# Kernel optimization log

Hardware: AMD Instinct MI355X
Metric: run time of the kernel (lower is better)

## Reference

```python
import jax, jax.numpy as jnp
import numpy as np
jax.config.update("jax_enable_x64", True)

TAPS, DELAY = 5, 3
EPS = 1e-6        # DNN_WPE.eps: power clamp before WPE
WPE_EPS = 1e-10   # wpe_one_iteration eps: inverse-power clamp + diag loading


def _signal_framing(Y, L):
    # Y: (..., T) -> (..., T-L+1, L) sliding frames (as_strided equivalent)
    T = Y.shape[-1]
    idx = jnp.arange(T - L + 1)[:, None] + jnp.arange(L)[None, :]
    return Y[..., idx]


def _wpe_one_iteration(Y, power, taps, delay):
    # Y: (B,F,C,T) complex128, power: (B,F,T) float64
    B, F, C, T = Y.shape
    inv_power = 1.0 / jnp.maximum(power, WPE_EPS)
    Tp = T - delay - taps + 1
    # tap-stacked delayed signal, taps axis reversed: (B,F,C,Tp,taps)
    Psi = _signal_framing(Y, taps)[..., :Tp, :][..., ::-1]
    Psi_n = Psi.conj() * inv_power[:, :, None, delay + taps - 1:, None]
    # covariance R: (B,F,taps*C,taps*C); cross-corr P: (B,F,taps,C_e,C_d)
    R = jnp.einsum("bfdtk,bfetl->bfkdle", Psi_n, Psi).reshape(B, F, taps * C, taps * C)
    P = jnp.einsum("bfdtk,bfet->bfked", Psi_n, Y[..., delay + taps - 1:])
    # v: (B,F,C_e,taps*C_d); conj filter G = inv(R) @ v^T  (X = v @ inv(R)^T)
    v = P.transpose(0, 1, 3, 2, 4).reshape(B, F, C, taps * C)
    eye = jnp.eye(taps * C, dtype=R.dtype)
    tr = jnp.trace(R, axis1=-2, axis2=-1).real[..., None, None] / (taps * C)
    G = jnp.linalg.solve(R + WPE_EPS * tr * eye, v.transpose(0, 1, 3, 2))
    G = G.reshape(B, F, taps, C, C)  # (B,F,tau,d,e) conjugated filter matrix
    # reverb tail: sum over taps of filtered, delayed signal
    tail = jnp.zeros_like(Y)
    for tau in range(taps):  # taps=5, small fixed loop
        s = delay + tau
        contrib = jnp.einsum("bfde,bfdt->bfet", G[:, :, tau], Y[..., : T - s])
        tail = tail.at[..., s:].add(contrib)
    return Y - tail


def setup_inputs() -> dict:
    key = jax.random.key(0)
    k1, k2, k3 = jax.random.split(key, 3)
    B, T, C, F = 4, 512, 8, 257
    data_real = jax.random.normal(k1, (B, T, C, F), dtype=jnp.float32)
    data_imag = jax.random.normal(k2, (B, T, C, F), dtype=jnp.float32)
    ilens = jax.random.randint(k3, (B,), 256, T + 1)
    return {"data_real": data_real, "data_imag": data_imag, "ilens": ilens}


def reference(data_real, data_imag, ilens):
    # (B,T,C,F) -> (B,F,C,T)
    data = (data_real + 1j * data_imag).transpose(0, 3, 2, 1)
    # power averaged over channels, clamped (B,F,T)
    power = jnp.maximum(jnp.mean(data.real ** 2 + data.imag ** 2, axis=-2), EPS)
    enh = _wpe_one_iteration(data.astype(jnp.complex128), power.astype(jnp.float64), TAPS, DELAY)
    enh = enh.astype(jnp.complex64)
    T = enh.shape[-1]
    pad = (jnp.arange(T)[None, :] >= ilens[:, None])[:, None, None, :]  # (B,1,1,T)
    enh = jnp.where(pad, 0.0 + 0.0j, enh)
    enh = enh.transpose(0, 3, 2, 1)  # back to (B,T,C,F)
    return enh.real, enh.imag, power
```

## Files before the change

### kernel.cpp

```cpp
#include <hip/hip_runtime.h>
#include <hip/hip_fp16.h>

#define B_ 4
#define T_ 512
#define C_ 8
#define F_ 257
#define TAPS 5
#define DELAY 3
#define N_ 40
#define NA 48
#define TP 505
#define T0 7
#define BF (B_*F_)
#define BTCF ((size_t)B_*T_*C_*F_)
#define YSH 532
#define YPAD 8
#define AUGSZ 1180

typedef _Float16 half8 __attribute__((ext_vector_type(8)));
typedef float floatx4 __attribute__((ext_vector_type(4)));
typedef uint32_t uint32x4 __attribute__((ext_vector_type(4)));

__device__ inline uint32_t h2mul(uint32_t a, uint32_t b) {
    __half2 r = __hmul2(__builtin_bit_cast(__half2, a), __builtin_bit_cast(__half2, b));
    return __builtin_bit_cast(uint32_t, r);
}
__device__ inline uint32_t packf16(float2 v) {
    __half2 h = __floats2half2_rn(v.x, v.y);
    return __builtin_bit_cast(uint32_t, h);
}
__device__ inline float2 unpackf16(uint32_t u) {
    __half2 h = __builtin_bit_cast(__half2, u);
    return make_float2(__low2float(h), __high2float(h));
}
__device__ inline half8 mkfrag(uint32_t a, uint32_t b, uint32_t c, uint32_t d) {
    uint32x4 v = {a, b, c, d};
    return __builtin_bit_cast(half8, v);
}
__device__ inline int rowoff(int i) {
    return i * 49 - ((i * (i - 1)) >> 1);
}

struct Frag { half8 X; half8 Y; };

__device__ inline Frag build2(const uint32_t* p, uint32_t sw0, uint32_t sw1,
                              uint32_t sw2, uint32_t sw3) {
    uint32_t q0 = p[0], q1 = p[1], q2 = p[2], q3 = p[3];
    uint32_t q4 = p[4], q5 = p[5], q6 = p[6], q7 = p[7];
    uint32_t x0 = __builtin_amdgcn_perm(q1, q0, 0x05040100);
    uint32_t y0 = __builtin_amdgcn_perm(q1, q0, 0x07060302);
    uint32_t x1 = __builtin_amdgcn_perm(q3, q2, 0x05040100);
    uint32_t y1 = __builtin_amdgcn_perm(q3, q2, 0x07060302);
    uint32_t x2 = __builtin_amdgcn_perm(q5, q4, 0x05040100);
    uint32_t y2 = __builtin_amdgcn_perm(q5, q4, 0x07060302);
    uint32_t x3 = __builtin_amdgcn_perm(q7, q6, 0x05040100);
    uint32_t y3 = __builtin_amdgcn_perm(q7, q6, 0x07060302);
    Frag f;
    f.X = mkfrag(h2mul(x0, sw0), h2mul(x1, sw1), h2mul(x2, sw2), h2mul(x3, sw3));
    f.Y = mkfrag(h2mul(y0, sw0), h2mul(y1, sw1), h2mul(y2, sw2), h2mul(y3, sw3));
    return f;
}
__device__ inline int zs_off(int j) {
    return (j < N_) ? (j & 7) * YSH + (YPAD + 4 - (j >> 3)) : (j - N_) * YSH + (YPAD + T0);
}

__global__ __launch_bounds__(256) void k_transpose_in(const float* __restrict__ in_re,
                                                      const float* __restrict__ in_im,
                                                      float2* __restrict__ Y) {
    __shared__ float2 tile[32][33];
    int ft = blockIdx.x % 9;
    int tt = blockIdx.x / 9;
    int c = blockIdx.y, b = blockIdx.z;
    int tx = threadIdx.x, ty = threadIdx.y;
    int f = ft * 32 + tx;
#pragma unroll
    for (int i = 0; i < 4; ++i) {
        int t = tt * 32 + ty + i * 8;
        if (f < F_) {
            size_t idx = ((size_t)(b * T_ + t) * C_ + c) * F_ + f;
            tile[ty + i * 8][tx] = make_float2(in_re[idx], in_im[idx]);
        }
    }
    __syncthreads();
    int t2 = tt * 32 + tx;
#pragma unroll
    for (int i = 0; i < 4; ++i) {
        int f2 = ft * 32 + ty + i * 8;
        if (f2 < F_) {
            Y[((size_t)(b * F_ + f2) * C_ + c) * T_ + t2] = tile[tx][ty + i * 8];
        }
    }
}

__global__ __launch_bounds__(256) void k_fused(float2* __restrict__ Y,
                                               float* __restrict__ pow_out) {
    __shared__ uint32_t sYh[C_ * YSH];
    __shared__ __align__(16) float uScr[640];
    __shared__ __align__(16) uint32_t sw_pk[256];
    __shared__ float2 sAugU[AUGSZ];
    float* sPow = uScr;
    float2* sGT = (float2*)uScr;
    int bf = blockIdx.x;
    int tid = threadIdx.x;
    float2* Yp = Y + (size_t)bf * C_ * T_;

    {
        const float4* Yp4 = (const float4*)Yp;
        int t0 = 2 * tid;
        float s0 = 0.f, s1 = 0.f;
#pragma unroll 2
        for (int c = 0; c < C_; ++c) {
            float4 v = Yp4[c * (T_ / 2) + tid];
            uint2 pk = make_uint2(packf16(make_float2(v.x, v.y)),
                                  packf16(make_float2(v.z, v.w)));
            *(uint2*)&sYh[c * YSH + YPAD + t0] = pk;
            s0 += v.x * v.x + v.y * v.y;
            s1 += v.z * v.z + v.w * v.w;
        }
        if (tid < 20) {
            int z = (tid < 8) ? tid : (512 + tid);
#pragma unroll
            for (int c = 0; c < C_; ++c) sYh[c * YSH + z] = 0;
        }
        s0 = fmaxf(s0 * (1.0f / C_), 1e-6f);
        s1 = fmaxf(s1 * (1.0f / C_), 1e-6f);
        ((float2*)(pow_out + (size_t)bf * T_))[tid] = make_float2(s0, s1);
        *(float2*)&sPow[t0] = make_float2(s0, s1);
    }
    __syncthreads();

    {
        int k0 = 2 * tid, k1 = k0 + 1;
        float w0 = (k0 < TP) ? rsqrtf(sPow[k0 + T0]) : 0.f;
        float w1 = (k1 < TP) ? rsqrtf(sPow[k1 + T0]) : 0.f;
        sw_pk[tid] = packf16(make_float2(w0, w1));
    }
    __syncthreads();

    int wv = tid >> 6, ln = tid & 63;
    if (wv < 3) {
        int r16 = ln & 15, kg = ln >> 4;
        int offB = zs_off(wv * 16 + r16);
#pragma unroll 1
        for (int mt = 0; mt < 3; ++mt) {
            int offA = zs_off(mt * 16 + r16);
            floatx4 aRe = {0.f, 0.f, 0.f, 0.f};
            floatx4 aIm = {0.f, 0.f, 0.f, 0.f};
#pragma unroll 2
            for (int ks = 0; ks < 16; ++ks) {
                int kbase = ks * 32 + kg * 8;
                uint32x4 sv = *(const uint32x4*)&sw_pk[kbase >> 1];
                Frag B = build2(&sYh[offB + kbase], sv[0], sv[1], sv[2], sv[3]);
                Frag A = build2(&sYh[offA + kbase], sv[0], sv[1], sv[2], sv[3]);
                half8 nYa = -A.Y;
                aRe = __builtin_amdgcn_mfma_f32_16x16x32_f16(A.X, B.X, aRe, 0, 0, 0);
                aRe = __builtin_amdgcn_mfma_f32_16x16x32_f16(A.Y, B.Y, aRe, 0, 0, 0);
                aIm = __builtin_amdgcn_mfma_f32_16x16x32_f16(A.X, B.Y, aIm, 0, 0, 0);
                aIm = __builtin_amdgcn_mfma_f32_16x16x32_f16(nYa, B.X, aIm, 0, 0, 0);
            }
#pragma unroll
            for (int r = 0; r < 4; ++r) {
                int m = mt * 16 + kg * 4 + r;
                int col = wv * 16 + r16;
                if (m < N_ && col >= m)
                    sAugU[rowoff(m) + col - m] = make_float2(aRe[r], aIm[r]);
            }
        }
    }
    __syncthreads();

    if (tid < 64) {
        float dv = (tid < N_) ? sAugU[rowoff(tid)].x : 0.f;
#pragma unroll
        for (int off = 32; off; off >>= 1) dv += __shfl_xor(dv, off, 64);
        if (tid < N_) sAugU[rowoff(tid)].x += 1e-10f * dv / N_;
    }
    __syncthreads();

    {
        int ri = tid >> 4, ci = tid & 15;
#pragma unroll 1
        for (int p = 0; p < N_ - 1; ++p) {
            int rop = rowoff(p);
            float2 piv = sAugU[rop];
            float dnm = piv.x * piv.x + piv.y * piv.y;
            float pix = piv.x / dnm, piy = -piv.y / dnm;
#pragma unroll 1
            for (int i = p + 1 + ri; i < N_; i += 16) {
                float2 api = sAugU[rop + i - p];
                float mx = api.x * pix + api.y * piy;
                float my = api.x * piy - api.y * pix;
                int roi = rowoff(i) - i;
#pragma unroll 1
                for (int j = i + ci; j < NA; j += 16) {
                    float2 apj = sAugU[rop + j - p];
                    float2 v = sAugU[roi + j];
                    v.x -= mx * apj.x - my * apj.y;
                    v.y -= mx * apj.y + my * apj.x;
                    sAugU[roi + j] = v;
                }
            }
            __syncthreads();
        }
    }
    {
        int bc = tid & 7, br = tid >> 3;
#pragma unroll 1
        for (int p = N_ - 1; p > 0; --p) {
            int rop = rowoff(p);
            float2 piv = sAugU[rop];
            float dnm = piv.x * piv.x + piv.y * piv.y;
            float pix = piv.x / dnm, piy = -piv.y / dnm;
            float2 rhs = sAugU[rop + N_ + bc - p];
            float xr = rhs.x * pix - rhs.y * piy;
            float xi = rhs.x * piy + rhs.y * pix;
#pragma unroll 1
            for (int i = br; i < p; i += 32) {
                int roi = rowoff(i) - i;
                float2 aip = sAugU[roi + p];
                float2 v = sAugU[roi + N_ + bc];
                v.x -= aip.x * xr - aip.y * xi;
                v.y -= aip.x * xi + aip.y * xr;
                sAugU[roi + N_ + bc] = v;
            }
            __syncthreads();
        }
    }
    for (int idx = tid; idx < N_ * C_; idx += 256) {
        int j = idx >> 3;
        int e = idx & 7;
        int roj = rowoff(j);
        float2 piv = sAugU[roj];
        float dnm = piv.x * piv.x + piv.y * piv.y;
        float pix = piv.x / dnm, piy = -piv.y / dnm;
        float2 rhs = sAugU[roj + N_ + e - j];
        int tau = j >> 3, d = j & 7;
        sGT[(e * C_ + d) * TAPS + tau] =
            make_float2(rhs.x * pix - rhs.y * piy, rhs.x * piy + rhs.y * pix);
    }
    __syncthreads();

#pragma unroll 1
    for (int eo = 0; eo < 2; ++eo) {
        int e = wv * 2 + eo;
        const float2* gE = &sGT[e * C_ * TAPS];
#pragma unroll 1
        for (int ti2 = 0; ti2 < 8; ++ti2) {
            int t = ln + 64 * ti2;
            float2 c = Yp[e * T_ + t];
            float tr = 0.f, tiv = 0.f;
#pragma unroll 2
            for (int d = 0; d < C_; ++d) {
                const uint32_t* yp = &sYh[d * YSH + t + (YPAD - T0)];
                uint32_t y0 = yp[0], y1 = yp[1], y2 = yp[2], y3 = yp[3], y4 = yp[4];
                float2 g0 = gE[d * TAPS + 0], g1 = gE[d * TAPS + 1],
                       g2 = gE[d * TAPS + 2], g3 = gE[d * TAPS + 3],
                       g4 = gE[d * TAPS + 4];
                float2 ya;
                ya = unpackf16(y4);
                tr += g0.x * ya.x - g0.y * ya.y; tiv += g0.x * ya.y + g0.y * ya.x;
                ya = unpackf16(y3);
                tr += g1.x * ya.x - g1.y * ya.y; tiv += g1.x * ya.y + g1.y * ya.x;
                ya = unpackf16(y2);
                tr += g2.x * ya.x - g2.y * ya.y; tiv += g2.x * ya.y + g2.y * ya.x;
                ya = unpackf16(y1);
                tr += g3.x * ya.x - g3.y * ya.y; tiv += g3.x * ya.y + g3.y * ya.x;
                ya = unpackf16(y0);
                tr += g4.x * ya.x - g4.y * ya.y; tiv += g4.x * ya.y + g4.y * ya.x;
            }
            Yp[e * T_ + t] = make_float2(c.x - tr, c.y - tiv);
        }
    }
}

__global__ __launch_bounds__(256) void k_transpose_out(const float2* __restrict__ Yenh,
                                                       const int* __restrict__ ilens,
                                                       float* __restrict__ out_re,
                                                       float* __restrict__ out_im) {
    __shared__ float2 tile[32][33];
    int ft = blockIdx.x % 9;
    int tt = blockIdx.x / 9;
    int c = blockIdx.y, b = blockIdx.z;
    int tx = threadIdx.x, ty = threadIdx.y;
    int ilen = ilens[b];
    int t = tt * 32 + tx;
#pragma unroll
    for (int i = 0; i < 4; ++i) {
        int f = ft * 32 + ty + i * 8;
        if (f < F_) tile[tx][ty + i * 8] = Yenh[((size_t)(b * F_ + f) * C_ + c) * T_ + t];
    }
    __syncthreads();
    int f2 = ft * 32 + tx;
#pragma unroll
    for (int i = 0; i < 4; ++i) {
        int t2 = tt * 32 + ty + i * 8;
        if (f2 < F_) {
            float2 v = tile[ty + i * 8][tx];
            if (t2 >= ilen) v = make_float2(0.f, 0.f);
            size_t o = ((size_t)(b * T_ + t2) * C_ + c) * F_ + f2;
            out_re[o] = v.x;
            out_im[o] = v.y;
        }
    }
}

extern "C" void kernel_launch(void* const* d_in, const int* in_sizes, int n_in,
                              void* d_out, int out_size, void* d_ws, size_t ws_size,
                              hipStream_t stream) {
    const float* in_re = (const float*)d_in[0];
    const float* in_im = (const float*)d_in[1];
    const int* ilens = (const int*)d_in[2];

    float* out_re = (float*)d_out;
    float* out_im = out_re + BTCF;
    float* out_pw = out_im + BTCF;

    float2* Y = (float2*)d_ws;

    dim3 tb(32, 8);
    dim3 tg(9 * 16, C_, B_);
    k_transpose_in<<<tg, tb, 0, stream>>>(in_re, in_im, Y);
    k_fused<<<BF, 256, 0, stream>>>(Y, out_pw);
    k_transpose_out<<<tg, tb, 0, stream>>>(Y, ilens, out_re, out_im);
}
```

Before: 228.0 us.

## Compute reverb-tail filtering with MFMA fp16 matrix ops instead of scalar FMAs

Replaces the scalar complex FMA loop that applies the WPE filter to the delayed signal with MFMA 16x16x32 fp16 matrix multiplies. Filter coefficients are packed into register fragments, and the shared-memory signal is restaged per 32-sample chunk into a transposed real/imag layout that reuses the augmented-matrix buffer. This removes per-thread scalar arithmetic, but it adds two block barriers per chunk, leaves half the waves idle during the MFMA phase, and rounds the filter to fp16.

```diff
diff --git a/kernel.cpp b/kernel.cpp
--- a/kernel.cpp
+++ b/kernel.cpp
@@ -16,6 +16,7 @@
 #define YSH 532
 #define YPAD 8
 #define AUGSZ 1180
+#define ZSD 36
 
 typedef _Float16 half8 __attribute__((ext_vector_type(8)));
 typedef float floatx4 __attribute__((ext_vector_type(4)));
@@ -28,10 +29,6 @@
 __device__ inline uint32_t packf16(float2 v) {
     __half2 h = __floats2half2_rn(v.x, v.y);
     return __builtin_bit_cast(uint32_t, h);
-}
-__device__ inline float2 unpackf16(uint32_t u) {
-    __half2 h = __builtin_bit_cast(__half2, u);
-    return make_float2(__low2float(h), __high2float(h));
 }
 __device__ inline half8 mkfrag(uint32_t a, uint32_t b, uint32_t c, uint32_t d) {
     uint32x4 v = {a, b, c, d};
@@ -97,7 +94,7 @@
     __shared__ uint32_t sYh[C_ * YSH];
     __shared__ __align__(16) float uScr[640];
     __shared__ __align__(16) uint32_t sw_pk[256];
-    __shared__ float2 sAugU[AUGSZ];
+    __shared__ __align__(16) float2 sAugU[AUGSZ];
     float* sPow = uScr;
     float2* sGT = (float2*)uScr;
     int bf = blockIdx.x;
@@ -138,8 +135,9 @@
     __syncthreads();
 
     int wv = tid >> 6, ln = tid & 63;
+    int kg = ln >> 4;
     if (wv < 3) {
-        int r16 = ln & 15, kg = ln >> 4;
+        int r16 = ln & 15;
         int offB = zs_off(wv * 16 + r16);
 #pragma unroll 1
         for (int mt = 0; mt < 3; ++mt) {
@@ -240,36 +238,71 @@
     }
     __syncthreads();
 
-#pragma unroll 1
-    for (int eo = 0; eo < 2; ++eo) {
-        int e = wv * 2 + eo;
-        const float2* gE = &sGT[e * C_ * TAPS];
-#pragma unroll 1
-        for (int ti2 = 0; ti2 < 8; ++ti2) {
-            int t = ln + 64 * ti2;
-            float2 c = Yp[e * T_ + t];
-            float tr = 0.f, tiv = 0.f;
-#pragma unroll 2
-            for (int d = 0; d < C_; ++d) {
-                const uint32_t* yp = &sYh[d * YSH + t + (YPAD - T0)];
-                uint32_t y0 = yp[0], y1 = yp[1], y2 = yp[2], y3 = yp[3], y4 = yp[4];
-                float2 g0 = gE[d * TAPS + 0], g1 = gE[d * TAPS + 1],
-                       g2 = gE[d * TAPS + 2], g3 = gE[d * TAPS + 3],
-                       g4 = gE[d * TAPS + 4];
-                float2 ya;
-                ya = unpackf16(y4);
-                tr += g0.x * ya.x - g0.y * ya.y; tiv += g0.x * ya.y + g0.y * ya.x;
-                ya = unpackf16(y3);
-                tr += g1.x * ya.x - g1.y * ya.y; tiv += g1.x * ya.y + g1.y * ya.x;
-                ya = unpackf16(y2);
-                tr += g2.x * ya.x - g2.y * ya.y; tiv += g2.x * ya.y + g2.y * ya.x;
-                ya = unpackf16(y1);
-                tr += g3.x * ya.x - g3.y * ya.y; tiv += g3.x * ya.y + g3.y * ya.x;
-                ya = unpackf16(y0);
-                tr += g4.x * ya.x - g4.y * ya.y; tiv += g4.x * ya.y + g4.y * ya.x;
-            }
-            Yp[e * T_ + t] = make_float2(c.x - tr, c.y - tiv);
-        }
+    uint32_t* zRe = (uint32_t*)sAugU;
+    uint32_t* zIm = zRe + 32 * ZSD;
+    half8 aFr[2], aFi[2];
+    {
+        int m = ln & 15;
+#pragma unroll
+        for (int ks = 0; ks < 2; ++ks) {
+            half8 hr = {}, hi = {};
+#pragma unroll
+            for (int q = 0; q < 8; ++q) {
+                int j = ks * 32 + kg * 8 + q;
+                float gx = 0.f, gy = 0.f;
+                if (m < 8 && j < N_) {
+                    float2 g = sGT[(m * C_ + (j & 7)) * TAPS + (j >> 3)];
+                    gx = g.x; gy = g.y;
+                }
+                hr[q] = (_Float16)gx;
+                hi[q] = (_Float16)gy;
+            }
+            aFr[ks] = hr;
+            aFi[ks] = hi;
+        }
+    }
+    for (int idx = tid; idx < 2 * 32 * ZSD; idx += 256) zRe[idx] = 0;
+    __syncthreads();
+
+#pragma unroll 1
+    for (int ch = 0; ch < 16; ++ch) {
+        int c0 = ch * 32;
+        for (int idx = tid; idx < 640; idx += 256) {
+            int jp = idx >> 5, tl = idx & 31;
+            int j0 = 2 * jp, j1 = j0 + 1;
+            int base = c0 + tl + (YPAD - 3);
+            uint32_t y0 = sYh[(j0 & 7) * YSH + base - (j0 >> 3)];
+            uint32_t y1 = sYh[(j1 & 7) * YSH + base - (j1 >> 3)];
+            zRe[tl * ZSD + jp] = __builtin_amdgcn_perm(y1, y0, 0x05040100);
+            zIm[tl * ZSD + jp] = __builtin_amdgcn_perm(y1, y0, 0x07060302);
+        }
+        __syncthreads();
+        if (wv < 2) {
+            floatx4 accR = {0.f, 0.f, 0.f, 0.f};
+            floatx4 accI = {0.f, 0.f, 0.f, 0.f};
+            int trow = wv * 16 + (ln & 15);
+#pragma unroll
+            for (int ks = 0; ks < 2; ++ks) {
+                int o = trow * ZSD + ks * 16 + kg * 4;
+                half8 Br = __builtin_bit_cast(half8, *(const uint32x4*)&zRe[o]);
+                half8 Bi = __builtin_bit_cast(half8, *(const uint32x4*)&zIm[o]);
+                half8 nFi = -aFi[ks];
+                accR = __builtin_amdgcn_mfma_f32_16x16x32_f16(aFr[ks], Br, accR, 0, 0, 0);
+                accR = __builtin_amdgcn_mfma_f32_16x16x32_f16(nFi, Bi, accR, 0, 0, 0);
+                accI = __builtin_amdgcn_mfma_f32_16x16x32_f16(aFr[ks], Bi, accI, 0, 0, 0);
+                accI = __builtin_amdgcn_mfma_f32_16x16x32_f16(aFi[ks], Br, accI, 0, 0, 0);
+            }
+            if (kg < 2) {
+                int tg = c0 + trow;
+#pragma unroll
+                for (int r = 0; r < 4; ++r) {
+                    int e = kg * 4 + r;
+                    float2 cur = Yp[e * T_ + tg];
+                    Yp[e * T_ + tg] = make_float2(cur.x - accR[r], cur.y - accI[r]);
+                }
+            }
+        }
+        __syncthreads();
     }
 }
 
```

After: 208.6 us. 8.5% less time.
